# Kernel optimization log

Hardware: AMD Instinct MI355X
Metric: run time of the kernel (lower is better)

The kernel has to match this reference:

```python
import jax, jax.numpy as jnp
import numpy as np


def setup_inputs() -> dict:
    key = jax.random.key(0)
    kq, kk, kv, km = jax.random.split(key, 4)
    B, H, S, D = 2, 16, 2048, 64
    queries = jax.random.normal(kq, (B, H, S, D), dtype=jnp.float32)
    keys = jax.random.normal(kk, (B, H, S, D), dtype=jnp.float32)
    values = jax.random.normal(kv, (B, H, S, D), dtype=jnp.float32)
    # additive binary mask (1 = masked position), broadcast over batch/heads
    mask = jax.random.randint(km, (1, 1, S, S), 0, 2, dtype=jnp.int32)
    return {"queries": queries, "keys": keys, "values": values,
            "mask": mask, "key_dim": D}


def reference(queries, keys, values, mask, key_dim):
    # scores = Q K^T / sqrt(d)   -> [B, H, S, S]
    scale = 1.0 / jnp.sqrt(jnp.asarray(key_dim, dtype=jnp.float32))
    scores = jnp.einsum('bhqd,bhkd->bhqk', queries, keys) * scale
    # additive mask: masked positions get -1e9
    scores = scores + (-1.0e9) * mask.astype(scores.dtype)
    weights = jax.nn.softmax(scores, axis=-1)
    # attention output: weights @ V -> [B, H, S, D]
    return jnp.einsum('bhqk,bhkd->bhqd', weights, values)
```

## Files before the change

kernel.cpp:

```cpp
#include <hip/hip_runtime.h>

typedef __attribute__((ext_vector_type(8))) short short8;
typedef __attribute__((ext_vector_type(4))) float floatx4;
typedef __attribute__((ext_vector_type(4))) unsigned short ushort4v;

#define S_LEN 2048
#define D_HEAD 64
#define NT64 (S_LEN / 64)
#define PITCH 72
#define TP 73
#define SCALE2 0.18033688f
#define MASK_BIAS2 -2.0e9f

static __device__ __forceinline__ unsigned short f2bf(float f) {
  unsigned int x = __builtin_bit_cast(unsigned int, f);
  x += 0x7fffu + ((x >> 16) & 1u);
  return (unsigned short)(x >> 16);
}
static __device__ __forceinline__ float bf2f(unsigned short u) {
  unsigned int x = ((unsigned int)u) << 16;
  return __builtin_bit_cast(float, x);
}
static __device__ __forceinline__ short8 cvt8(const float* __restrict__ p) {
  float4 a = *(const float4*)p;
  float4 b = *(const float4*)(p + 4);
  short8 r;
  r[0] = (short)f2bf(a.x); r[1] = (short)f2bf(a.y);
  r[2] = (short)f2bf(a.z); r[3] = (short)f2bf(a.w);
  r[4] = (short)f2bf(b.x); r[5] = (short)f2bf(b.y);
  r[6] = (short)f2bf(b.z); r[7] = (short)f2bf(b.w);
  return r;
}
static __device__ __forceinline__ short8 cvt8s(const float* __restrict__ p) {
  float4 a = *(const float4*)p;
  float4 b = *(const float4*)(p + 4);
  short8 r;
  r[0] = (short)f2bf(a.x * SCALE2); r[1] = (short)f2bf(a.y * SCALE2);
  r[2] = (short)f2bf(a.z * SCALE2); r[3] = (short)f2bf(a.w * SCALE2);
  r[4] = (short)f2bf(b.x * SCALE2); r[5] = (short)f2bf(b.y * SCALE2);
  r[6] = (short)f2bf(b.z * SCALE2); r[7] = (short)f2bf(b.w * SCALE2);
  return r;
}
static __device__ __forceinline__ void cp16(const void* g, void* l) {
  __builtin_amdgcn_global_load_lds(
      (const __attribute__((address_space(1))) unsigned int*)g,
      (__attribute__((address_space(3))) unsigned int*)l, 16, 0, 0);
}
static __device__ __forceinline__ unsigned int pk2(float a, float b) {
  return (unsigned int)f2bf(a) | ((unsigned int)f2bf(b) << 16);
}

__global__ __launch_bounds__(256) void prep(
    const float* __restrict__ K, const float* __restrict__ V,
    const int* __restrict__ mask,
    unsigned short* __restrict__ Kws, unsigned short* __restrict__ Vws,
    unsigned long long* __restrict__ Mb, int BH)
{
  __shared__ unsigned short t[D_HEAD * TP];
  const int tid = threadIdx.x;
  const int nbK = BH * 64;
  const int nbV = BH * 32;
  int b = blockIdx.x;

  if (b < nbK) {
    const int tt   = b * 256 + tid;
    const int bh   = tt >> 14;
    const int rem  = tt & 16383;
    const int tile = rem >> 9;
    const int n    = rem & 511;
    const int row  = n >> 3;
    const int col8 = (n & 7) ^ (row & 7);
    short8 r = cvt8(K + ((size_t)(bh * S_LEN + tile * 64 + row)) * D_HEAD + col8 * 8);
    *(short8*)(Kws + (size_t)tt * 8) = r;
    return;
  }
  b -= nbK;
  if (b < nbV) {
    const int tile = b & 31;
    const int bh   = b >> 5;
    const int s0   = tile * 64;
    const float* Vb = V + (size_t)bh * S_LEN * D_HEAD;
#pragma unroll
    for (int p = 0; p < 4; ++p) {
      const int s  = p * 16 + (tid >> 4);
      const int d0 = (tid & 15) * 4;
      float4 v = *(const float4*)(Vb + (size_t)(s0 + s) * D_HEAD + d0);
      unsigned short* dst = &t[s * TP + d0];
      dst[0] = f2bf(v.x); dst[1] = f2bf(v.y); dst[2] = f2bf(v.z); dst[3] = f2bf(v.w);
    }
    __syncthreads();
    unsigned short* Vo = Vws + ((size_t)(bh * 32 + tile)) * 4096;
#pragma unroll
    for (int p = 0; p < 2; ++p) {
      const int n    = p * 256 + tid;
      const int d    = n >> 3;
      const int col8 = (n & 7) ^ (d & 7);
      short8 r;
#pragma unroll
      for (int j = 0; j < 8; ++j) r[j] = (short)t[(col8 * 8 + j) * TP + d];
      *(short8*)(Vo + (size_t)n * 8) = r;
    }
    return;
  }
  b -= nbV;
  const int lane = tid & 63;
  const int row  = b * 4 + (tid >> 6);
#pragma unroll 4
  for (int c = 0; c < NT64; ++c) {
    const int mv = mask[(size_t)row * S_LEN + c * 64 + lane];
    const unsigned long long bm = __ballot(mv != 0);
    if (lane == 0) Mb[(size_t)row * NT64 + c] = bm;
  }
}

__global__ __launch_bounds__(256, 3) void fa_fwd6(
    const float* __restrict__ Q,
    const unsigned short* __restrict__ Kws,
    const unsigned short* __restrict__ Vws,
    const unsigned long long* __restrict__ Mb,
    float* __restrict__ Out)
{
  __shared__ unsigned short Kbuf[2][64 * 64];
  __shared__ unsigned short Vbuf[2][64 * 64];
  __shared__ unsigned short Plds[4][32 * 64];

  const int tid  = threadIdx.x;
  const int wv   = tid >> 6;
  const int lane = tid & 63;
  const int quad = lane >> 4;
  const int l16  = lane & 15;
  const int l8   = l16 & 7;

  const int bh = blockIdx.y;
  const int qw = blockIdx.x * 128 + wv * 32;

  const float* Qb = Q + (size_t)bh * S_LEN * D_HEAD;
  const unsigned short* KT = Kws + (size_t)bh * NT64 * 4096;
  const unsigned short* VT = Vws + (size_t)bh * NT64 * 4096;

  short8 qfrag[2][2];
#pragma unroll
  for (int g = 0; g < 2; ++g)
#pragma unroll
    for (int w = 0; w < 2; ++w)
      qfrag[g][w] = cvt8s(Qb + (size_t)(qw + g * 16 + l16) * D_HEAD + w * 32 + quad * 8);

  floatx4 ot[2][4];
#pragma unroll
  for (int g = 0; g < 2; ++g)
#pragma unroll
    for (int dt = 0; dt < 4; ++dt) ot[g][dt] = (floatx4){0.f, 0.f, 0.f, 0.f};
  float lsum[2] = {0.f, 0.f};

  unsigned short* pl = &Plds[wv][0];
  const unsigned long long* mrowp[2];
#pragma unroll
  for (int g = 0; g < 2; ++g)
    mrowp[g] = Mb + (size_t)(qw + g * 16 + l16) * NT64;

  auto stage = [&](int kt, int buf) {
#pragma unroll
    for (int j = 0; j < 2; ++j) {
      const int c0 = (wv * 2 + j) * 64;
      cp16(KT + (size_t)kt * 4096 + (size_t)(c0 + lane) * 8, &Kbuf[buf][c0 * 8]);
      cp16(VT + (size_t)kt * 4096 + (size_t)(c0 + lane) * 8, &Vbuf[buf][c0 * 8]);
    }
  };

  stage(0, 0);
  __syncthreads();

  for (int kt = 0; kt < NT64; ++kt) {
    const int cur = kt & 1;
    if (kt + 1 < NT64) stage(kt + 1, cur ^ 1);
    const unsigned short* Kl = Kbuf[cur];
    const unsigned short* Vl = Vbuf[cur];

    floatx4 st[2][4];
#pragma unroll
    for (int g = 0; g < 2; ++g)
#pragma unroll
      for (int nt = 0; nt < 4; ++nt) st[g][nt] = (floatx4){0.f, 0.f, 0.f, 0.f};
#pragma unroll
    for (int w = 0; w < 2; ++w)
#pragma unroll
      for (int nt = 0; nt < 4; ++nt) {
        short8 kf = *(const short8*)&Kl[(nt * 16 + l16) * 64 + (((w * 4 + quad) ^ l8) * 8)];
        st[0][nt] = __builtin_amdgcn_mfma_f32_16x16x32_bf16(kf, qfrag[0][w], st[0][nt], 0, 0, 0);
        st[1][nt] = __builtin_amdgcn_mfma_f32_16x16x32_bf16(kf, qfrag[1][w], st[1][nt], 0, 0, 0);
      }

#pragma unroll
    for (int g = 0; g < 2; ++g) {
      const unsigned long long mw = mrowp[g][kt];
#pragma unroll
      for (int nt = 0; nt < 4; ++nt) {
        const unsigned nib = (unsigned)(mw >> (nt * 16 + quad * 4)) & 0xFu;
        float p[4];
#pragma unroll
        for (int r = 0; r < 4; ++r) {
          float pv = __builtin_amdgcn_exp2f(st[g][nt][r]);
          pv = ((nib >> r) & 1u) ? 0.0f : pv;
          lsum[g] += pv;
          p[r] = pv;
        }
        const unsigned int d0 = pk2(p[0], p[1]);
        const unsigned int d1 = pk2(p[2], p[3]);
        const int c = nt * 2 + (quad >> 1);
        unsigned int* dst = (unsigned int*)&pl[(g * 16 + l16) * 64 + ((c ^ l8) * 8) + (quad & 1) * 4];
        dst[0] = d0; dst[1] = d1;
      }
    }

#pragma unroll
    for (int w = 0; w < 2; ++w) {
      short8 pf0 = *(const short8*)&pl[(l16) * 64 + (((w * 4 + quad) ^ l8) * 8)];
      short8 pf1 = *(const short8*)&pl[(16 + l16) * 64 + (((w * 4 + quad) ^ l8) * 8)];
#pragma unroll
      for (int dt = 0; dt < 4; ++dt) {
        short8 vf = *(const short8*)&Vl[(dt * 16 + l16) * 64 + (((w * 4 + quad) ^ l8) * 8)];
        ot[0][dt] = __builtin_amdgcn_mfma_f32_16x16x32_bf16(vf, pf0, ot[0][dt], 0, 0, 0);
        ot[1][dt] = __builtin_amdgcn_mfma_f32_16x16x32_bf16(vf, pf1, ot[1][dt], 0, 0, 0);
      }
    }
    __syncthreads();
  }

#pragma unroll
  for (int g = 0; g < 2; ++g) {
    float l = lsum[g];
    l += __shfl_xor(l, 16);
    l += __shfl_xor(l, 32);
    const float invl = 1.0f / l;
    float* Ob = Out + (size_t)bh * S_LEN * D_HEAD + (size_t)(qw + g * 16 + l16) * D_HEAD;
#pragma unroll
    for (int dt = 0; dt < 4; ++dt) {
      float4 v;
      v.x = ot[g][dt][0] * invl; v.y = ot[g][dt][1] * invl;
      v.z = ot[g][dt][2] * invl; v.w = ot[g][dt][3] * invl;
      *(float4*)(Ob + dt * 16 + quad * 4) = v;
    }
  }
}

__global__ __launch_bounds__(256) void fa_fwd(
    const float* __restrict__ Q, const float* __restrict__ K, const float* __restrict__ V,
    const int* __restrict__ mask, float* __restrict__ Out)
{
  __shared__ unsigned short Vt[D_HEAD * PITCH];
  __shared__ unsigned short Plds[4][16 * PITCH];
  const int tid = threadIdx.x, wv = tid >> 6, lane = tid & 63, quad = lane >> 4, l16 = lane & 15;
  const int bh = blockIdx.y, qw = blockIdx.x * 64 + wv * 16;
  const float* Qb = Q + (size_t)bh * S_LEN * D_HEAD;
  const float* Kb = K + (size_t)bh * S_LEN * D_HEAD;
  const float* Vb = V + (size_t)bh * S_LEN * D_HEAD;
  short8 qfrag[2];
#pragma unroll
  for (int w = 0; w < 2; ++w)
    qfrag[w] = cvt8(Qb + (size_t)(qw + l16) * D_HEAD + w * 32 + quad * 8);
  floatx4 o[4];
#pragma unroll
  for (int nt = 0; nt < 4; ++nt) o[nt] = (floatx4){0.f, 0.f, 0.f, 0.f};
  float m_run[4], l_run[4];
#pragma unroll
  for (int r = 0; r < 4; ++r) { m_run[r] = -1.0e30f; l_run[r] = 0.f; }
  unsigned short* pl = &Plds[wv][0];
  for (int kt = 0; kt < NT64; ++kt) {
    const int k0 = kt * 64;
    __syncthreads();
#pragma unroll
    for (int it = 0; it < 2; ++it) {
      const int s = it * 32 + (tid >> 3), d0 = (tid & 7) * 8, dblk = (tid & 7);
      const int swz = (((s >> 3) ^ dblk) & 7) * 8 + (s & 7);
      const float* vp = Vb + (size_t)(k0 + s) * D_HEAD + d0;
      float4 a = *(const float4*)vp; float4 bb = *(const float4*)(vp + 4);
      const float vvv[8] = {a.x, a.y, a.z, a.w, bb.x, bb.y, bb.z, bb.w};
#pragma unroll
      for (int j = 0; j < 8; ++j) Vt[(d0 + j) * PITCH + swz] = f2bf(vvv[j]);
    }
    __syncthreads();
    floatx4 scf[4];
#pragma unroll
    for (int nt = 0; nt < 4; ++nt) scf[nt] = (floatx4){0.f, 0.f, 0.f, 0.f};
#pragma unroll
    for (int w = 0; w < 2; ++w)
#pragma unroll
      for (int nt = 0; nt < 4; ++nt) {
        short8 kf = cvt8(Kb + (size_t)(k0 + nt * 16 + l16) * D_HEAD + w * 32 + quad * 8);
        scf[nt] = __builtin_amdgcn_mfma_f32_16x16x32_bf16(qfrag[w], kf, scf[nt], 0, 0, 0);
      }
    float s_val[4][4], mloc[4] = {-1.0e30f, -1.0e30f, -1.0e30f, -1.0e30f};
#pragma unroll
    for (int nt = 0; nt < 4; ++nt)
#pragma unroll
      for (int r = 0; r < 4; ++r) {
        const int mk = mask[(size_t)(qw + quad * 4 + r) * S_LEN + (k0 + nt * 16 + l16)];
        const float sv = scf[nt][r] * SCALE2 + (mk ? MASK_BIAS2 : 0.0f);
        s_val[nt][r] = sv; mloc[r] = fmaxf(mloc[r], sv);
      }
#pragma unroll
    for (int r = 0; r < 4; ++r)
#pragma unroll
      for (int off = 1; off < 16; off <<= 1) mloc[r] = fmaxf(mloc[r], __shfl_xor(mloc[r], off));
    float alpha[4], rsum[4];
#pragma unroll
    for (int r = 0; r < 4; ++r) {
      const float mnew = fmaxf(m_run[r], mloc[r]);
      alpha[r] = exp2f(m_run[r] - mnew); m_run[r] = mnew; rsum[r] = 0.f;
    }
#pragma unroll
    for (int nt = 0; nt < 4; ++nt)
#pragma unroll
      for (int r = 0; r < 4; ++r) {
        const float p = exp2f(s_val[nt][r] - m_run[r]);
        const unsigned short ph = f2bf(p);
        rsum[r] += bf2f(ph);
        pl[(quad * 4 + r) * PITCH + nt * 16 + l16] = ph;
      }
    __syncthreads();
#pragma unroll
    for (int r = 0; r < 4; ++r) {
#pragma unroll
      for (int off = 1; off < 16; off <<= 1) rsum[r] += __shfl_xor(rsum[r], off);
      l_run[r] = l_run[r] * alpha[r] + rsum[r];
    }
#pragma unroll
    for (int nt = 0; nt < 4; ++nt)
#pragma unroll
      for (int r = 0; r < 4; ++r) o[nt][r] *= alpha[r];
#pragma unroll
    for (int w = 0; w < 2; ++w) {
      short8 af = *(const short8*)&pl[l16 * PITCH + w * 32 + quad * 8];
#pragma unroll
      for (int nt = 0; nt < 4; ++nt) {
        const int d = nt * 16 + l16, blk = ((w * 4 + quad) ^ (d >> 3)) & 7;
        short8 vf = *(const short8*)&Vt[d * PITCH + blk * 8];
        o[nt] = __builtin_amdgcn_mfma_f32_16x16x32_bf16(af, vf, o[nt], 0, 0, 0);
      }
    }
  }
  float invl[4];
#pragma unroll
  for (int r = 0; r < 4; ++r) invl[r] = 1.0f / l_run[r];
  float* Ob = Out + (size_t)bh * S_LEN * D_HEAD;
#pragma unroll
  for (int nt = 0; nt < 4; ++nt)
#pragma unroll
    for (int r = 0; r < 4; ++r)
      Ob[(size_t)(qw + quad * 4 + r) * D_HEAD + nt * 16 + l16] = o[nt][r] * invl[r];
}

extern "C" void kernel_launch(void* const* d_in, const int* in_sizes, int n_in,
                              void* d_out, int out_size, void* d_ws, size_t ws_size,
                              hipStream_t stream) {
  const float* Q = (const float*)d_in[0];
  const float* K = (const float*)d_in[1];
  const float* V = (const float*)d_in[2];
  const int* mask = (const int*)d_in[3];
  float* Out = (float*)d_out;
  const int BH = in_sizes[0] / (S_LEN * D_HEAD);
  const size_t NH = (size_t)BH * S_LEN * D_HEAD;
  const size_t nMb = (size_t)S_LEN * NT64;
  const size_t need = NH * 2 * 2 + nMb * 8;

  if (ws_size >= need) {
    unsigned short* Kws = (unsigned short*)d_ws;
    unsigned short* Vws = Kws + NH;
    unsigned long long* Mbits = (unsigned long long*)(Vws + NH);
    const int nbPrep = BH * 64 + BH * 32 + S_LEN / 4;
    prep<<<dim3(nbPrep), 256, 0, stream>>>(K, V, mask, Kws, Vws, Mbits, BH);
    fa_fwd6<<<dim3(S_LEN / 128, BH), 256, 0, stream>>>(Q, Kws, Vws, Mbits, Out);
  } else {
    fa_fwd<<<dim3(S_LEN / 64, BH), 256, 0, stream>>>(Q, K, V, mask, Out);
  }
}
```

Baseline: 181.9 us.

## Compute softmax row sums via MFMA with ones, cheaper bf16 pack, split mask prep

The softmax denominator is now accumulated by an extra MFMA that multiplies the bf16 probability tile by a vector of ones, replacing the per-element scalar adds and the final cross-lane shuffles. The float-to-bf16 pack switches from round-to-nearest-even to a round-half-up add plus a byte-permute instruction. The mask bit-packing part of the prep kernel is split across four times as many blocks, each handling eight column tiles, for more parallelism. The row sum now adds up the bf16-rounded probabilities, which matches the values fed to the PV product, and the rounding mode differs slightly from before.

```diff
diff --git a/kernel.cpp b/kernel.cpp
--- a/kernel.cpp
+++ b/kernel.cpp
@@ -46,8 +46,10 @@
       (const __attribute__((address_space(1))) unsigned int*)g,
       (__attribute__((address_space(3))) unsigned int*)l, 16, 0, 0);
 }
-static __device__ __forceinline__ unsigned int pk2(float a, float b) {
-  return (unsigned int)f2bf(a) | ((unsigned int)f2bf(b) << 16);
+static __device__ __forceinline__ unsigned int pk2f(float a, float b) {
+  const unsigned int ab = __builtin_bit_cast(unsigned int, a) + 0x8000u;
+  const unsigned int bb = __builtin_bit_cast(unsigned int, b) + 0x8000u;
+  return __builtin_amdgcn_perm(bb, ab, 0x07060302u);
 }
 
 __global__ __launch_bounds__(256) void prep(
@@ -103,17 +105,19 @@
     return;
   }
   b -= nbV;
+  const int rg   = b >> 2;
+  const int cq   = b & 3;
   const int lane = tid & 63;
-  const int row  = b * 4 + (tid >> 6);
-#pragma unroll 4
-  for (int c = 0; c < NT64; ++c) {
+  const int row  = rg * 4 + (tid >> 6);
+#pragma unroll 8
+  for (int c = cq * 8; c < cq * 8 + 8; ++c) {
     const int mv = mask[(size_t)row * S_LEN + c * 64 + lane];
     const unsigned long long bm = __ballot(mv != 0);
     if (lane == 0) Mb[(size_t)row * NT64 + c] = bm;
   }
 }
 
-__global__ __launch_bounds__(256, 3) void fa_fwd6(
+__global__ __launch_bounds__(256, 3) void fa_fwd9(
     const float* __restrict__ Q,
     const unsigned short* __restrict__ Kws,
     const unsigned short* __restrict__ Vws,
@@ -145,12 +149,18 @@
     for (int w = 0; w < 2; ++w)
       qfrag[g][w] = cvt8s(Qb + (size_t)(qw + g * 16 + l16) * D_HEAD + w * 32 + quad * 8);
 
+  short8 kones;
+#pragma unroll
+  for (int j = 0; j < 8; ++j) kones[j] = (short)0x3F80;
+
   floatx4 ot[2][4];
 #pragma unroll
   for (int g = 0; g < 2; ++g)
 #pragma unroll
     for (int dt = 0; dt < 4; ++dt) ot[g][dt] = (floatx4){0.f, 0.f, 0.f, 0.f};
-  float lsum[2] = {0.f, 0.f};
+  floatx4 lacc[2];
+  lacc[0] = (floatx4){0.f, 0.f, 0.f, 0.f};
+  lacc[1] = (floatx4){0.f, 0.f, 0.f, 0.f};
 
   unsigned short* pl = &Plds[wv][0];
   const unsigned long long* mrowp[2];
@@ -200,12 +210,10 @@
 #pragma unroll
         for (int r = 0; r < 4; ++r) {
           float pv = __builtin_amdgcn_exp2f(st[g][nt][r]);
-          pv = ((nib >> r) & 1u) ? 0.0f : pv;
-          lsum[g] += pv;
-          p[r] = pv;
+          p[r] = ((nib >> r) & 1u) ? 0.0f : pv;
         }
-        const unsigned int d0 = pk2(p[0], p[1]);
-        const unsigned int d1 = pk2(p[2], p[3]);
+        const unsigned int d0 = pk2f(p[0], p[1]);
+        const unsigned int d1 = pk2f(p[2], p[3]);
         const int c = nt * 2 + (quad >> 1);
         unsigned int* dst = (unsigned int*)&pl[(g * 16 + l16) * 64 + ((c ^ l8) * 8) + (quad & 1) * 4];
         dst[0] = d0; dst[1] = d1;
@@ -216,6 +224,8 @@
     for (int w = 0; w < 2; ++w) {
       short8 pf0 = *(const short8*)&pl[(l16) * 64 + (((w * 4 + quad) ^ l8) * 8)];
       short8 pf1 = *(const short8*)&pl[(16 + l16) * 64 + (((w * 4 + quad) ^ l8) * 8)];
+      lacc[0] = __builtin_amdgcn_mfma_f32_16x16x32_bf16(kones, pf0, lacc[0], 0, 0, 0);
+      lacc[1] = __builtin_amdgcn_mfma_f32_16x16x32_bf16(kones, pf1, lacc[1], 0, 0, 0);
 #pragma unroll
       for (int dt = 0; dt < 4; ++dt) {
         short8 vf = *(const short8*)&Vl[(dt * 16 + l16) * 64 + (((w * 4 + quad) ^ l8) * 8)];
@@ -228,10 +238,7 @@
 
 #pragma unroll
   for (int g = 0; g < 2; ++g) {
-    float l = lsum[g];
-    l += __shfl_xor(l, 16);
-    l += __shfl_xor(l, 32);
-    const float invl = 1.0f / l;
+    const float invl = 1.0f / lacc[g][0];
     float* Ob = Out + (size_t)bh * S_LEN * D_HEAD + (size_t)(qw + g * 16 + l16) * D_HEAD;
 #pragma unroll
     for (int dt = 0; dt < 4; ++dt) {
@@ -367,9 +374,9 @@
     unsigned short* Kws = (unsigned short*)d_ws;
     unsigned short* Vws = Kws + NH;
     unsigned long long* Mbits = (unsigned long long*)(Vws + NH);
-    const int nbPrep = BH * 64 + BH * 32 + S_LEN / 4;
+    const int nbPrep = BH * 64 + BH * 32 + S_LEN;
     prep<<<dim3(nbPrep), 256, 0, stream>>>(K, V, mask, Kws, Vws, Mbits, BH);
-    fa_fwd6<<<dim3(S_LEN / 128, BH), 256, 0, stream>>>(Q, Kws, Vws, Mbits, Out);
+    fa_fwd9<<<dim3(S_LEN / 128, BH), 256, 0, stream>>>(Q, Kws, Vws, Mbits, Out);
   } else {
     fa_fwd<<<dim3(S_LEN / 64, BH), 256, 0, stream>>>(Q, K, V, mask, Out);
   }
```

Result: faster. 168.1 us (-7.6%).
